# Optimization experiments

Measured on AMD Instinct MI355X. Metric: run time of the kernel, lower is better.

## Reference

```python
import jax, jax.numpy as jnp
import numpy as np

H = 16  # num_heads (matches init_kwargs)
MASK_VAL = -10000.0


def setup_inputs() -> dict:
    key = jax.random.key(0)
    k1, k2, k3, k4, k5 = jax.random.split(key, 5)
    B, N, C = 2, 2048, 1024
    hidden_states = jax.random.normal(k1, (B, N, C), dtype=jnp.float32)
    encoder_hidden_states = jax.random.normal(k2, (B, N, C), dtype=jnp.float32)
    pad_mask = jax.random.bernoulli(k3, 0.1, (B, N))
    # Linear weights stored as (in, out); scaled ~Xavier so softmax isn't saturated
    W_q = jax.random.normal(k4, (C, C), dtype=jnp.float32) * (C ** -0.5)
    W_c = jax.random.normal(k5, (C, 2 * C), dtype=jnp.float32) * (C ** -0.5)
    return {"hidden_states": hidden_states,
            "encoder_hidden_states": encoder_hidden_states,
            "pad_mask": pad_mask,
            "W_q": W_q,
            "W_c": W_c}


def _split_heads(x, B, N, C):
    # (B, N, C) -> (B, H, N, D)
    return x.reshape(B, N, H, C // H).transpose(0, 2, 1, 3)


def reference(hidden_states, encoder_hidden_states, pad_mask, W_q, W_c):
    B, N, C = hidden_states.shape
    D = C // H
    scaler = D ** -0.5

    q = hidden_states @ W_q                       # (B, N, C)
    kv = encoder_hidden_states @ W_c              # (B, N, 2C)
    k, v = kv[..., :C], kv[..., C:]

    q = _split_heads(q, B, N, C)                  # (B, H, N, D)
    k = _split_heads(k, B, N, C)
    v = _split_heads(v, B, N, C)

    scores = jnp.einsum('bhid,bhjd->bhij', q, k) * scaler  # (B, H, N, N)

    # construct_mask: expanded[b,i,j] = pad_mask[b,i] OR pad_mask[b,j]
    expanded = pad_mask[:, None, :, None] | pad_mask[:, None, None, :]
    scores = jnp.where(expanded, MASK_VAL, scores)

    # max-subtract + softmax (dropout_rate=0 so dropout is identity)
    scores = scores - jax.lax.stop_gradient(scores.max(axis=-1, keepdims=True))
    att_weights = jax.nn.softmax(scores, axis=-1)

    att = jnp.einsum('bhij,bhjd->bhid', att_weights, v)   # (B, H, N, D)
    att = att.transpose(0, 2, 1, 3).reshape(B, N, C)
    return att, att_weights
```

## Files before the change

### kernel.cpp

```cpp
#include <hip/hip_runtime.h>
#include <math.h>

#define B_ 2
#define N_ 2048
#define C_ 1024
#define H_ 16
#define D_ 64

typedef __attribute__((ext_vector_type(8))) short short8v;
typedef __attribute__((ext_vector_type(4))) short short4v;
typedef __attribute__((ext_vector_type(4))) float f32x4;

static __device__ __forceinline__ short f2bf(float f) {
    union { float f; unsigned u; } v; v.f = f;
    unsigned r = v.u + 0x7FFFu + ((v.u >> 16) & 1u);
    return (short)(r >> 16);
}

static __device__ __forceinline__ void splitbf(float f, short& h, short& l) {
    union { float f; unsigned u; } v; v.f = f;
    const unsigned uh = v.u & 0xFFFF0000u;
    h = (short)(uh >> 16);
    union { unsigned u; float f; } w; w.u = uh;
    union { float f; unsigned u; } x; x.f = f - w.f;
    l = (short)(x.u >> 16);
}

#define GKSTR 40

__global__ __launch_bounds__(256) void gemm_x3(const float* __restrict__ A,
                                               const float* __restrict__ Bm,
                                               short* __restrict__ Cm,
                                               int K, int N) {
    __shared__ __align__(16) short Ahi[128][GKSTR];
    __shared__ __align__(16) short Alo[128][GKSTR];
    __shared__ __align__(16) short Bhi[64][GKSTR];
    __shared__ __align__(16) short Blo[64][GKSTR];

    const int t  = threadIdx.x;
    const int w  = t >> 6;
    const int l  = t & 63;
    const int lq = l & 15;
    const int hq = l >> 4;
    const int wr = w >> 1;
    const int wc = w & 1;
    const int m0 = blockIdx.y * 128;
    const int n0 = blockIdx.x * 64;

    const int arow = t >> 3;
    const int akc  = (t & 7) * 4;
    const int bn   = t & 63;
    const int bkq  = w * 8;

    f32x4 acc[4][2];
#pragma unroll
    for (int mi = 0; mi < 4; ++mi)
#pragma unroll
        for (int ni = 0; ni < 2; ++ni) acc[mi][ni] = (f32x4){0.f, 0.f, 0.f, 0.f};

    for (int k0 = 0; k0 < K; k0 += 32) {
        float4 af[4];
#pragma unroll
        for (int it = 0; it < 4; ++it)
            af[it] = *(const float4*)&A[(size_t)(m0 + arow + it * 32) * K + k0 + akc];
        float bf[8];
#pragma unroll
        for (int kk = 0; kk < 8; ++kk)
            bf[kk] = Bm[(size_t)(k0 + bkq + kk) * N + n0 + bn];

        short4v ah[4], al[4];
#pragma unroll
        for (int it = 0; it < 4; ++it) {
            short h, lo2;
            splitbf(af[it].x, h, lo2); ah[it][0] = h; al[it][0] = lo2;
            splitbf(af[it].y, h, lo2); ah[it][1] = h; al[it][1] = lo2;
            splitbf(af[it].z, h, lo2); ah[it][2] = h; al[it][2] = lo2;
            splitbf(af[it].w, h, lo2); ah[it][3] = h; al[it][3] = lo2;
        }
        short8v bh, bl;
#pragma unroll
        for (int kk = 0; kk < 8; ++kk) {
            short h, lo2;
            splitbf(bf[kk], h, lo2); bh[kk] = h; bl[kk] = lo2;
        }

        __syncthreads();
#pragma unroll
        for (int it = 0; it < 4; ++it) {
            *(short4v*)&Ahi[arow + it * 32][akc] = ah[it];
            *(short4v*)&Alo[arow + it * 32][akc] = al[it];
        }
        *(short8v*)&Bhi[bn][bkq] = bh;
        *(short8v*)&Blo[bn][bkq] = bl;
        __syncthreads();

        short8v amh[4], aml[4], bnh[2], bnl[2];
#pragma unroll
        for (int mi = 0; mi < 4; ++mi) {
            amh[mi] = *(const short8v*)&Ahi[wr * 64 + mi * 16 + lq][hq * 8];
            aml[mi] = *(const short8v*)&Alo[wr * 64 + mi * 16 + lq][hq * 8];
        }
#pragma unroll
        for (int ni = 0; ni < 2; ++ni) {
            bnh[ni] = *(const short8v*)&Bhi[wc * 32 + ni * 16 + lq][hq * 8];
            bnl[ni] = *(const short8v*)&Blo[wc * 32 + ni * 16 + lq][hq * 8];
        }
#pragma unroll
        for (int mi = 0; mi < 4; ++mi)
#pragma unroll
            for (int ni = 0; ni < 2; ++ni) {
                acc[mi][ni] = __builtin_amdgcn_mfma_f32_16x16x32_bf16(amh[mi], bnh[ni], acc[mi][ni], 0, 0, 0);
                acc[mi][ni] = __builtin_amdgcn_mfma_f32_16x16x32_bf16(amh[mi], bnl[ni], acc[mi][ni], 0, 0, 0);
                acc[mi][ni] = __builtin_amdgcn_mfma_f32_16x16x32_bf16(aml[mi], bnh[ni], acc[mi][ni], 0, 0, 0);
            }
    }

#pragma unroll
    for (int mi = 0; mi < 4; ++mi)
#pragma unroll
        for (int ni = 0; ni < 2; ++ni) {
            const int col = n0 + wc * 32 + ni * 16 + lq;
#pragma unroll
            for (int r = 0; r < 4; ++r) {
                const int row = m0 + wr * 64 + mi * 16 + hq * 4 + r;
                Cm[(size_t)row * N + col] = f2bf(acc[mi][ni][r]);
            }
        }
}

__global__ __launch_bounds__(256) void v_transpose(const short* __restrict__ kv_bf,
                                                   short* __restrict__ vt) {
    __shared__ __align__(16) short Ls[128][72];
    const int t  = threadIdx.x;
    const int jt = blockIdx.x * 128;
    const int h  = blockIdx.y;
    const int b  = blockIdx.z;
    const short* src = kv_bf + (size_t)b * N_ * 2 * C_ + C_ + h * D_;
#pragma unroll
    for (int it = 0; it < 4; ++it) {
        const int idx = it * 256 + t;
        const int j = idx >> 3, d0 = (idx & 7) * 8;
        *(short8v*)&Ls[j][d0] = *(const short8v*)&src[(size_t)(jt + j) * (2 * C_) + d0];
    }
    __syncthreads();
    short* dst = vt + ((size_t)(b * H_ + h)) * D_ * N_;
#pragma unroll
    for (int it = 0; it < 4; ++it) {
        const int idx = it * 256 + t;
        const int d  = idx >> 4;
        const int j0 = (idx & 15) * 8;
        short8v s;
#pragma unroll
        for (int jj = 0; jj < 8; ++jj) s[jj] = Ls[j0 + jj][d];
        *(short8v*)&dst[(size_t)d * N_ + jt + j0] = s;
    }
}

#define KSTR 72
#define VSTR 136
#define PSTR 136

__global__ __launch_bounds__(256) void attn_mfma(const short* __restrict__ q,
                                                 const short* __restrict__ kv,
                                                 const short* __restrict__ vtg,
                                                 const int* __restrict__ mask,
                                                 float* __restrict__ out_att,
                                                 float* __restrict__ out_w) {
    __shared__ __align__(16) short Ks[128][KSTR];
    __shared__ __align__(16) short Vt[64][VSTR];
    __shared__ __align__(16) short Ps[4][16][PSTR];
    __shared__ float linv_s[4][16];
    __shared__ int   mcol_s[128];

    const int t  = threadIdx.x;
    const int w  = t >> 6;
    const int l  = t & 63;
    const int lq = l & 15;
    const int hq = l >> 4;

    const int qb = blockIdx.x;
    const int h  = blockIdx.y;
    const int b  = blockIdx.z;
    const int i0 = qb * 64 + w * 16;

    short8v qa[2];
    {
        const short* qrow = q + ((size_t)(b * N_ + i0 + lq)) * C_ + h * D_;
        qa[0] = *(const short8v*)&qrow[hq * 8];
        qa[1] = *(const short8v*)&qrow[32 + hq * 8];
    }

    int mr[4];
#pragma unroll
    for (int r = 0; r < 4; ++r) mr[r] = mask[b * N_ + i0 + hq * 4 + r];

    const short* kbase = kv + (size_t)b * N_ * 2 * C_ + h * D_;
    const short* vtb   = vtg + ((size_t)(b * H_ + h)) * D_ * N_;

    float lsum[4] = {0.f, 0.f, 0.f, 0.f};
    for (int tile = 0; tile < 16; ++tile) {
        const int jt = tile * 128;
        __syncthreads();
#pragma unroll
        for (int it = 0; it < 4; ++it) {
            const int idx = it * 256 + t;
            const int j = idx >> 3, d0 = (idx & 7) * 8;
            *(short8v*)&Ks[j][d0] = *(const short8v*)&kbase[(size_t)(jt + j) * (2 * C_) + d0];
        }
        if (t < 128) mcol_s[t] = mask[b * N_ + jt + t];
        __syncthreads();
#pragma unroll
        for (int cb = 0; cb < 8; ++cb) {
            f32x4 acc = {0.f, 0.f, 0.f, 0.f};
            const short8v b0 = *(short8v*)&Ks[cb * 16 + lq][hq * 8];
            const short8v b1 = *(short8v*)&Ks[cb * 16 + lq][32 + hq * 8];
            acc = __builtin_amdgcn_mfma_f32_16x16x32_bf16(qa[0], b0, acc, 0, 0, 0);
            acc = __builtin_amdgcn_mfma_f32_16x16x32_bf16(qa[1], b1, acc, 0, 0, 0);
            const int mc = mcol_s[cb * 16 + lq];
#pragma unroll
            for (int r = 0; r < 4; ++r)
                lsum[r] += mr[r] ? 1.0f : (mc ? 0.0f : __expf(acc[r] * 0.125f));
        }
    }
    float inv[4];
#pragma unroll
    for (int r = 0; r < 4; ++r) {
        float s = lsum[r];
#pragma unroll
        for (int off = 1; off < 16; off <<= 1) s += __shfl_xor(s, off, 64);
        inv[r] = 1.0f / s;
    }
    if (lq == 0)
#pragma unroll
        for (int r = 0; r < 4; ++r) linv_s[w][hq * 4 + r] = inv[r];

    float* wrow[4];
#pragma unroll
    for (int r = 0; r < 4; ++r)
        wrow[r] = out_w + ((size_t)((b * H_ + h) * N_ + i0 + hq * 4 + r)) * N_;

    f32x4 oacc[4];
#pragma unroll
    for (int db = 0; db < 4; ++db) oacc[db] = (f32x4){0.f, 0.f, 0.f, 0.f};

    for (int tile = 0; tile < 16; ++tile) {
        const int jt = tile * 128;
        __syncthreads();
#pragma unroll
        for (int it = 0; it < 4; ++it) {
            const int idx = it * 256 + t;
            const int j = idx >> 3, d0 = (idx & 7) * 8;
            *(short8v*)&Ks[j][d0] = *(const short8v*)&kbase[(size_t)(jt + j) * (2 * C_) + d0];
        }
#pragma unroll
        for (int it = 0; it < 4; ++it) {
            const int idx = it * 256 + t;
            const int d  = idx >> 4;
            const int j0 = (idx & 15) * 8;
            *(short8v*)&Vt[d][j0] = *(const short8v*)&vtb[(size_t)d * N_ + jt + j0];
        }
        if (t < 128) mcol_s[t] = mask[b * N_ + jt + t];
        __syncthreads();

#pragma unroll
        for (int cb = 0; cb < 8; ++cb) {
            f32x4 acc = {0.f, 0.f, 0.f, 0.f};
            const short8v b0 = *(short8v*)&Ks[cb * 16 + lq][hq * 8];
            const short8v b1 = *(short8v*)&Ks[cb * 16 + lq][32 + hq * 8];
            acc = __builtin_amdgcn_mfma_f32_16x16x32_bf16(qa[0], b0, acc, 0, 0, 0);
            acc = __builtin_amdgcn_mfma_f32_16x16x32_bf16(qa[1], b1, acc, 0, 0, 0);
            const int mc   = mcol_s[cb * 16 + lq];
            const int jcol = cb * 16 + lq;
#pragma unroll
            for (int r = 0; r < 4; ++r) {
                const float ev = mr[r] ? 1.0f : (mc ? 0.0f : __expf(acc[r] * 0.125f));
                wrow[r][jt + jcol] = ev * inv[r];
                Ps[w][hq * 4 + r][jcol] = f2bf(ev);
            }
        }
        __syncthreads();

#pragma unroll
        for (int db = 0; db < 4; ++db)
#pragma unroll
            for (int kb = 0; kb < 4; ++kb) {
                const short8v va = *(short8v*)&Vt[db * 16 + lq][kb * 32 + hq * 8];
                const short8v pb = *(short8v*)&Ps[w][lq][kb * 32 + hq * 8];
                oacc[db] = __builtin_amdgcn_mfma_f32_16x16x32_bf16(va, pb, oacc[db], 0, 0, 0);
            }
    }

    {
        const float invi = linv_s[w][lq];
        const size_t abase = ((size_t)(b * N_ + i0 + lq)) * C_ + h * D_;
#pragma unroll
        for (int db = 0; db < 4; ++db)
#pragma unroll
            for (int r = 0; r < 4; ++r)
                out_att[abase + db * 16 + hq * 4 + r] = oacc[db][r] * invi;
    }
}

extern "C" void kernel_launch(void* const* d_in, const int* in_sizes, int n_in,
                              void* d_out, int out_size, void* d_ws, size_t ws_size,
                              hipStream_t stream) {
    const float* hs   = (const float*)d_in[0];
    const float* ehs  = (const float*)d_in[1];
    const int*   mask = (const int*)d_in[2];
    const float* W_q  = (const float*)d_in[3];
    const float* W_c  = (const float*)d_in[4];

    float* out_att = (float*)d_out;
    float* out_w   = (float*)d_out + (size_t)B_ * N_ * C_;

    short* qbf  = (short*)d_ws;
    short* kvbf = qbf + (size_t)B_ * N_ * C_;
    short* vt   = kvbf + (size_t)B_ * N_ * 2 * C_;

    gemm_x3<<<dim3(C_ / 64, (B_ * N_) / 128), 256, 0, stream>>>(
        hs, W_q, qbf, C_, C_);
    gemm_x3<<<dim3((2 * C_) / 64, (B_ * N_) / 128), 256, 0, stream>>>(
        ehs, W_c, kvbf, C_, 2 * C_);
    v_transpose<<<dim3(N_ / 128, H_, B_), 256, 0, stream>>>(kvbf, vt);

    attn_mfma<<<dim3(N_ / 64, H_, B_), 256, 0, stream>>>(
        qbf, kvbf, vt, mask, out_att, out_w);
}
```

Measured before the change: 365.5 us.

## Prefetch next tiles into registers in GEMM and attention, swizzle attention grid

The GEMM loop and both attention passes now load the next K-tile (and the V and mask tiles) from global memory into registers while the current tile is being computed, so load latency overlaps MFMA work. The attention launch becomes a 1D grid with a swizzle that spreads consecutive blocks across (q-block, head, batch) groups, likely to improve L2 locality or balance across XCDs. The cost is higher register pressure from the prefetch buffers, which may reduce occupancy.

Measured after the change: 323.5 us. 11.5% less time.

```diff
diff --git a/kernel.cpp b/kernel.cpp
--- a/kernel.cpp
+++ b/kernel.cpp
@@ -58,32 +58,32 @@
 #pragma unroll
         for (int ni = 0; ni < 2; ++ni) acc[mi][ni] = (f32x4){0.f, 0.f, 0.f, 0.f};
 
+    float4 af[4];
+    float  bf[8];
+#pragma unroll
+    for (int it = 0; it < 4; ++it)
+        af[it] = *(const float4*)&A[(size_t)(m0 + arow + it * 32) * K + akc];
+#pragma unroll
+    for (int kk = 0; kk < 8; ++kk)
+        bf[kk] = Bm[(size_t)(bkq + kk) * N + n0 + bn];
+
+    short4v ah[4], al[4];
+    short8v bh, bl;
+#pragma unroll
+    for (int it = 0; it < 4; ++it) {
+        short h, lo2;
+        splitbf(af[it].x, h, lo2); ah[it][0] = h; al[it][0] = lo2;
+        splitbf(af[it].y, h, lo2); ah[it][1] = h; al[it][1] = lo2;
+        splitbf(af[it].z, h, lo2); ah[it][2] = h; al[it][2] = lo2;
+        splitbf(af[it].w, h, lo2); ah[it][3] = h; al[it][3] = lo2;
+    }
+#pragma unroll
+    for (int kk = 0; kk < 8; ++kk) {
+        short h, lo2;
+        splitbf(bf[kk], h, lo2); bh[kk] = h; bl[kk] = lo2;
+    }
+
     for (int k0 = 0; k0 < K; k0 += 32) {
-        float4 af[4];
-#pragma unroll
-        for (int it = 0; it < 4; ++it)
-            af[it] = *(const float4*)&A[(size_t)(m0 + arow + it * 32) * K + k0 + akc];
-        float bf[8];
-#pragma unroll
-        for (int kk = 0; kk < 8; ++kk)
-            bf[kk] = Bm[(size_t)(k0 + bkq + kk) * N + n0 + bn];
-
-        short4v ah[4], al[4];
-#pragma unroll
-        for (int it = 0; it < 4; ++it) {
-            short h, lo2;
-            splitbf(af[it].x, h, lo2); ah[it][0] = h; al[it][0] = lo2;
-            splitbf(af[it].y, h, lo2); ah[it][1] = h; al[it][1] = lo2;
-            splitbf(af[it].z, h, lo2); ah[it][2] = h; al[it][2] = lo2;
-            splitbf(af[it].w, h, lo2); ah[it][3] = h; al[it][3] = lo2;
-        }
-        short8v bh, bl;
-#pragma unroll
-        for (int kk = 0; kk < 8; ++kk) {
-            short h, lo2;
-            splitbf(bf[kk], h, lo2); bh[kk] = h; bl[kk] = lo2;
-        }
-
         __syncthreads();
 #pragma unroll
         for (int it = 0; it < 4; ++it) {
@@ -93,6 +93,16 @@
         *(short8v*)&Bhi[bn][bkq] = bh;
         *(short8v*)&Blo[bn][bkq] = bl;
         __syncthreads();
+
+        const int kn = k0 + 32;
+        if (kn < K) {
+#pragma unroll
+            for (int it = 0; it < 4; ++it)
+                af[it] = *(const float4*)&A[(size_t)(m0 + arow + it * 32) * K + kn + akc];
+#pragma unroll
+            for (int kk = 0; kk < 8; ++kk)
+                bf[kk] = Bm[(size_t)(kn + bkq + kk) * N + n0 + bn];
+        }
 
         short8v amh[4], aml[4], bnh[2], bnl[2];
 #pragma unroll
@@ -113,6 +123,22 @@
                 acc[mi][ni] = __builtin_amdgcn_mfma_f32_16x16x32_bf16(amh[mi], bnl[ni], acc[mi][ni], 0, 0, 0);
                 acc[mi][ni] = __builtin_amdgcn_mfma_f32_16x16x32_bf16(aml[mi], bnh[ni], acc[mi][ni], 0, 0, 0);
             }
+
+        if (kn < K) {
+#pragma unroll
+            for (int it = 0; it < 4; ++it) {
+                short h, lo2;
+                splitbf(af[it].x, h, lo2); ah[it][0] = h; al[it][0] = lo2;
+                splitbf(af[it].y, h, lo2); ah[it][1] = h; al[it][1] = lo2;
+                splitbf(af[it].z, h, lo2); ah[it][2] = h; al[it][2] = lo2;
+                splitbf(af[it].w, h, lo2); ah[it][3] = h; al[it][3] = lo2;
+            }
+#pragma unroll
+            for (int kk = 0; kk < 8; ++kk) {
+                short h, lo2;
+                splitbf(bf[kk], h, lo2); bh[kk] = h; bl[kk] = lo2;
+            }
+        }
     }
 
 #pragma unroll
@@ -178,10 +204,17 @@
     const int lq = l & 15;
     const int hq = l >> 4;
 
-    const int qb = blockIdx.x;
-    const int h  = blockIdx.y;
-    const int b  = blockIdx.z;
+    const int lin = blockIdx.x;
+    const int swz = (lin & 7) * 128 + (lin >> 3);
+    const int qb = swz & 31;
+    const int h  = (swz >> 5) & 15;
+    const int b  = swz >> 9;
     const int i0 = qb * 64 + w * 16;
+
+    const int sj = t >> 3;
+    const int sd = (t & 7) * 8;
+    const int vd = t >> 4;
+    const int vj = (t & 15) * 8;
 
     short8v qa[2];
     {
@@ -198,17 +231,29 @@
     const short* vtb   = vtg + ((size_t)(b * H_ + h)) * D_ * N_;
 
     float lsum[4] = {0.f, 0.f, 0.f, 0.f};
+    short8v kr[4];
+    int mpre = 0;
+#pragma unroll
+    for (int it = 0; it < 4; ++it)
+        kr[it] = *(const short8v*)&kbase[(size_t)(it * 32 + sj) * (2 * C_) + sd];
+    if (t < 128) mpre = mask[b * N_ + t];
+
     for (int tile = 0; tile < 16; ++tile) {
-        const int jt = tile * 128;
-        __syncthreads();
-#pragma unroll
-        for (int it = 0; it < 4; ++it) {
-            const int idx = it * 256 + t;
-            const int j = idx >> 3, d0 = (idx & 7) * 8;
-            *(short8v*)&Ks[j][d0] = *(const short8v*)&kbase[(size_t)(jt + j) * (2 * C_) + d0];
-        }
-        if (t < 128) mcol_s[t] = mask[b * N_ + jt + t];
-        __syncthreads();
+        __syncthreads();
+#pragma unroll
+        for (int it = 0; it < 4; ++it)
+            *(short8v*)&Ks[it * 32 + sj][sd] = kr[it];
+        if (t < 128) mcol_s[t] = mpre;
+        __syncthreads();
+
+        if (tile < 15) {
+            const int jn = (tile + 1) * 128;
+#pragma unroll
+            for (int it = 0; it < 4; ++it)
+                kr[it] = *(const short8v*)&kbase[(size_t)(jn + it * 32 + sj) * (2 * C_) + sd];
+            if (t < 128) mpre = mask[b * N_ + jn + t];
+        }
+
 #pragma unroll
         for (int cb = 0; cb < 8; ++cb) {
             f32x4 acc = {0.f, 0.f, 0.f, 0.f};
@@ -243,24 +288,34 @@
 #pragma unroll
     for (int db = 0; db < 4; ++db) oacc[db] = (f32x4){0.f, 0.f, 0.f, 0.f};
 
+    short8v vr[4];
+#pragma unroll
+    for (int it = 0; it < 4; ++it) {
+        kr[it] = *(const short8v*)&kbase[(size_t)(it * 32 + sj) * (2 * C_) + sd];
+        vr[it] = *(const short8v*)&vtb[(size_t)(it * 16 + vd) * N_ + vj];
+    }
+    if (t < 128) mpre = mask[b * N_ + t];
+
     for (int tile = 0; tile < 16; ++tile) {
         const int jt = tile * 128;
         __syncthreads();
 #pragma unroll
         for (int it = 0; it < 4; ++it) {
-            const int idx = it * 256 + t;
-            const int j = idx >> 3, d0 = (idx & 7) * 8;
-            *(short8v*)&Ks[j][d0] = *(const short8v*)&kbase[(size_t)(jt + j) * (2 * C_) + d0];
-        }
-#pragma unroll
-        for (int it = 0; it < 4; ++it) {
-            const int idx = it * 256 + t;
-            const int d  = idx >> 4;
-            const int j0 = (idx & 15) * 8;
-            *(short8v*)&Vt[d][j0] = *(const short8v*)&vtb[(size_t)d * N_ + jt + j0];
-        }
-        if (t < 128) mcol_s[t] = mask[b * N_ + jt + t];
-        __syncthreads();
+            *(short8v*)&Ks[it * 32 + sj][sd] = kr[it];
+            *(short8v*)&Vt[it * 16 + vd][vj] = vr[it];
+        }
+        if (t < 128) mcol_s[t] = mpre;
+        __syncthreads();
+
+        if (tile < 15) {
+            const int jn = jt + 128;
+#pragma unroll
+            for (int it = 0; it < 4; ++it) {
+                kr[it] = *(const short8v*)&kbase[(size_t)(jn + it * 32 + sj) * (2 * C_) + sd];
+                vr[it] = *(const short8v*)&vtb[(size_t)(it * 16 + vd) * N_ + jn + vj];
+            }
+            if (t < 128) mpre = mask[b * N_ + jn + t];
+        }
 
 #pragma unroll
         for (int cb = 0; cb < 8; ++cb) {
@@ -323,6 +378,6 @@
         ehs, W_c, kvbf, C_, 2 * C_);
     v_transpose<<<dim3(N_ / 128, H_, B_), 256, 0, stream>>>(kvbf, vt);
 
-    attn_mfma<<<dim3(N_ / 64, H_, B_), 256, 0, stream>>>(
+    attn_mfma<<<dim3(1024), 256, 0, stream>>>(
         qbf, kvbf, vt, mask, out_att, out_w);
 }
```
